# Kernel optimization log

Measured on AMD Instinct MI355X. Metric: run time of the kernel, lower is better.

The kernel has to match this reference:

```python
import jax, jax.numpy as jnp
import numpy as np

SCALE_EPS = 1e-05


def _qweight(weight):
    # global abs-mean scale (detached), round-to-nearest-even, clamp to {-1,0,1}
    scale = SCALE_EPS + jax.lax.stop_gradient(jnp.mean(jnp.abs(weight)))
    quant = jnp.clip(jnp.round(weight / scale), -1.0, 1.0)
    # straight-through estimator: forward = quant, backward = identity on weight
    return weight + jax.lax.stop_gradient(quant - weight)


def setup_inputs() -> dict:
    key = jax.random.key(0)
    k_x, k_w = jax.random.split(key)
    B, S, IN, OUT = 4, 2048, 2048, 8192
    x = jax.random.normal(k_x, (B, S, IN), dtype=jnp.float32)
    weight = jax.random.normal(k_w, (OUT, IN), dtype=jnp.float32)
    bias = jnp.zeros((OUT,), dtype=jnp.float32)
    return {"x": x, "weight": weight, "bias": bias}


def reference(x, weight, bias):
    qw = _qweight(weight)  # ternary-valued (scaled forward value)
    # F.linear: x @ qw.T + bias ; [b,s,in] x [out,in] -> [b,s,out]
    return jnp.einsum('bsi,oi->bso', x, qw) + bias
```

## Files before the change

kernel.cpp:

```cpp
#include <hip/hip_runtime.h>
#include <hip/hip_bf16.h>

typedef __attribute__((ext_vector_type(8))) short bf16x8;
typedef __attribute__((ext_vector_type(4))) float f32x4;

__device__ __forceinline__ unsigned short f2bf_rne(float f) {
  unsigned int u = __float_as_uint(f);
  u += 0x7FFFu + ((u >> 16) & 1u);
  return (unsigned short)(u >> 16);
}

__device__ __forceinline__ float bf2f(unsigned short h) {
  return __uint_as_float(((unsigned int)h) << 16);
}

__global__ void absmean_kernel(const float* __restrict__ w, long n, double* __restrict__ out) {
  double s = 0.0;
  long stride = (long)gridDim.x * blockDim.x * 4;
  for (long i = ((long)blockIdx.x * blockDim.x + threadIdx.x) * 4; i < n; i += stride) {
    float4 v = *(const float4*)(w + i);
    s += (double)fabsf(v.x) + (double)fabsf(v.y) + (double)fabsf(v.z) + (double)fabsf(v.w);
  }
  for (int o = 32; o > 0; o >>= 1) s += __shfl_down(s, o, 64);
  __shared__ double ls[4];
  int lane = threadIdx.x & 63, wv = threadIdx.x >> 6;
  if (lane == 0) ls[wv] = s;
  __syncthreads();
  if (threadIdx.x == 0) atomicAdd(out, ls[0] + ls[1] + ls[2] + ls[3]);
}

__global__ void prep_x_kernel(const float* __restrict__ x, unsigned short* __restrict__ xcat,
                              int kshift, long n) {
  const int K = 1 << kshift;
  long stride = (long)gridDim.x * blockDim.x * 4;
  for (long i = ((long)blockIdx.x * blockDim.x + threadIdx.x) * 4; i < n; i += stride) {
    float4 v = *(const float4*)(x + i);
    float f[4] = {v.x, v.y, v.z, v.w};
    unsigned short hi[4], lo[4];
#pragma unroll
    for (int j = 0; j < 4; ++j) {
      hi[j] = f2bf_rne(f[j]);
      lo[j] = f2bf_rne(f[j] - bf2f(hi[j]));
    }
    long row = i >> kshift;
    int col = (int)(i & (K - 1));
    unsigned short* p0 = xcat + (row << (kshift + 1)) + col;
    *(ushort4*)p0 = make_ushort4(hi[0], hi[1], hi[2], hi[3]);
    *(ushort4*)(p0 + K) = make_ushort4(lo[0], lo[1], lo[2], lo[3]);
  }
}

__global__ void prep_w_kernel(const float* __restrict__ w, unsigned short* __restrict__ wcat,
                              const double* __restrict__ sum, int kshift, long n,
                              double inv_cnt) {
  const int K = 1 << kshift;
  float scale = 1e-5f + (float)(*sum * inv_cnt);
  long stride = (long)gridDim.x * blockDim.x * 4;
  for (long i = ((long)blockIdx.x * blockDim.x + threadIdx.x) * 4; i < n; i += stride) {
    float4 v = *(const float4*)(w + i);
    float f[4] = {v.x, v.y, v.z, v.w};
    unsigned short q[4];
#pragma unroll
    for (int j = 0; j < 4; ++j) {
      float t = f[j] / scale;
      t = rintf(t);
      t = fminf(1.0f, fmaxf(-1.0f, t));
      q[j] = f2bf_rne(t);
    }
    long row = i >> kshift;
    int col = (int)(i & (K - 1));
    unsigned short* p0 = wcat + (row << (kshift + 1)) + col;
    *(ushort4*)p0 = make_ushort4(q[0], q[1], q[2], q[3]);
    *(ushort4*)(p0 + K) = make_ushort4(q[0], q[1], q[2], q[3]);
  }
}

__device__ __forceinline__ void gll16(const unsigned short* g, void* l) {
  __builtin_amdgcn_global_load_lds((const __attribute__((address_space(1))) unsigned int*)g,
                                   (__attribute__((address_space(3))) unsigned int*)l,
                                   16, 0, 0);
}

__global__ __launch_bounds__(512) void gemm8p_kernel(
    const unsigned short* __restrict__ A,
    const unsigned short* __restrict__ Bw,
    const float* __restrict__ bias,
    float* __restrict__ C, int M, int N) {
  constexpr int Kc = 4096;
  constexpr int NT = 128;
  __shared__ __align__(16) unsigned short lds[65536];

  const int nbx = N >> 8;
  const int nwg = (M >> 8) * nbx;
  const int q8 = nwg >> 3, r8 = nwg & 7;
  const int xcd = blockIdx.x & 7;
  const int loc = blockIdx.x >> 3;
  const int wgid = (xcd < r8 ? xcd * (q8 + 1) : r8 * (q8 + 1) + (xcd - r8) * q8) + loc;
  const int bx = wgid % nbx;
  const int by = wgid / nbx;
  const int bm = by << 8;
  const int bn = bx << 8;

  const int tid = threadIdx.x;
  const int lane = tid & 63;
  const int wid = tid >> 6;
  const int wr = wid >> 2;
  const int wc = wid & 3;

  f32x4 acc[8][4] = {};

  const int strow = tid >> 2;
  const int sslot = ((tid & 3) ^ ((tid >> 2) & 3)) * 8;
  const unsigned short* sA0 = A + (size_t)(bm + strow) * Kc + sslot;
  const unsigned short* sA1 = A + (size_t)(bm + 128 + strow) * Kc + sslot;
  const unsigned short* sB0 = Bw + (size_t)(bn + strow) * Kc + sslot;
  const unsigned short* sB1 = Bw + (size_t)(bn + 128 + strow) * Kc + sslot;
  char* dA = (char*)lds + (size_t)wid * 1024;
  char* dB = (char*)lds + 65536 + (size_t)wid * 1024;

  const int scol = (((lane >> 4) ^ (lane & 3)) << 3);
  const int aoff = (wr * 128 + (lane & 15)) * 32 + scol;
  const int boff = 32768 + (wc * 64 + (lane & 15)) * 32 + scol;

#pragma unroll
  for (int p = 0; p < 3; ++p) {
    gll16(sA0 + p * 32, dA + p * 16384);
    gll16(sA1 + p * 32, dA + p * 16384 + 8192);
    gll16(sB0 + p * 32, dB + p * 16384);
    gll16(sB1 + p * 32, dB + p * 16384 + 8192);
  }
  asm volatile("s_waitcnt vmcnt(8)" ::: "memory");
  __builtin_amdgcn_s_barrier();

  bf16x8 a_[4], b_[4];
  for (int t = 0; t < NT; ++t) {
    const unsigned short* base = lds + (t & 3) * 8192;
    const int sb = (t + 3) & 3;
    const int sk = (t + 3) * 32;
    const bool doStage = (t + 3) < NT;

#pragma unroll
    for (int mi = 0; mi < 4; ++mi)
      a_[mi] = *(const bf16x8*)&base[aoff + mi * 512];
#pragma unroll
    for (int ni = 0; ni < 4; ++ni)
      b_[ni] = *(const bf16x8*)&base[boff + ni * 512];
    if (doStage) {
      gll16(sA0 + sk, dA + sb * 16384);
      gll16(sA1 + sk, dA + sb * 16384 + 8192);
    }
    __builtin_amdgcn_s_barrier();
    asm volatile("s_waitcnt lgkmcnt(0)" ::: "memory");
    __builtin_amdgcn_sched_barrier(0);
    __builtin_amdgcn_s_setprio(1);
#pragma unroll
    for (int mi = 0; mi < 4; ++mi)
#pragma unroll
      for (int ni = 0; ni < 4; ++ni)
        acc[mi][ni] = __builtin_amdgcn_mfma_f32_16x16x32_bf16(a_[mi], b_[ni], acc[mi][ni], 0, 0, 0);
    __builtin_amdgcn_s_setprio(0);
    __builtin_amdgcn_s_barrier();

#pragma unroll
    for (int mi = 0; mi < 4; ++mi)
      a_[mi] = *(const bf16x8*)&base[aoff + (mi + 4) * 512];
    if (doStage) {
      gll16(sB0 + sk, dB + sb * 16384);
      gll16(sB1 + sk, dB + sb * 16384 + 8192);
    }
    __builtin_amdgcn_s_barrier();
    asm volatile("s_waitcnt lgkmcnt(0)" ::: "memory");
    __builtin_amdgcn_sched_barrier(0);
    __builtin_amdgcn_s_setprio(1);
#pragma unroll
    for (int mi = 0; mi < 4; ++mi)
#pragma unroll
      for (int ni = 0; ni < 4; ++ni)
        acc[mi + 4][ni] = __builtin_amdgcn_mfma_f32_16x16x32_bf16(a_[mi], b_[ni], acc[mi + 4][ni], 0, 0, 0);
    __builtin_amdgcn_s_setprio(0);
    if (t < NT - 3) {
      asm volatile("s_waitcnt vmcnt(8)" ::: "memory");
    } else if (t == NT - 3) {
      asm volatile("s_waitcnt vmcnt(4)" ::: "memory");
    } else if (t == NT - 2) {
      asm volatile("s_waitcnt vmcnt(0)" ::: "memory");
    }
    __builtin_amdgcn_s_barrier();
  }

  const int r0 = bm + wr * 128 + (lane >> 4) * 4;
  const int c0 = bn + wc * 64 + (lane & 15);
#pragma unroll
  for (int ni = 0; ni < 4; ++ni) {
    const int col = c0 + ni * 16;
    const float bv = bias[col];
#pragma unroll
    for (int mi = 0; mi < 8; ++mi) {
#pragma unroll
      for (int rr = 0; rr < 4; ++rr)
        C[(size_t)(r0 + mi * 16 + rr) * N + col] = acc[mi][ni][rr] + bv;
    }
  }
}

__global__ void fallback_kernel(const float* __restrict__ x, const float* __restrict__ w,
                                const float* __restrict__ bias, const double* __restrict__ sum,
                                float* __restrict__ out, int M, int N, int K, double inv_cnt) {
  float scale = 1e-5f + (float)(*sum * inv_cnt);
  __shared__ float xs[64][33];
  __shared__ float qs[64][33];
  const int tid = threadIdx.x;
  const int bm = blockIdx.y * 64, bn = blockIdx.x * 64;
  const int ty = tid >> 4, tx = tid & 15;
  float acc[4][4] = {};
  for (int k0 = 0; k0 < K; k0 += 32) {
    for (int p = 0; p < 8; ++p) {
      int idx = p * 256 + tid;
      int r = idx >> 5, c = idx & 31;
      xs[r][c] = x[(size_t)(bm + r) * K + k0 + c];
      float t = w[(size_t)(bn + r) * K + k0 + c] / scale;
      t = rintf(t);
      qs[r][c] = fminf(1.0f, fmaxf(-1.0f, t));
    }
    __syncthreads();
    for (int kk = 0; kk < 32; ++kk) {
      float a[4], b[4];
#pragma unroll
      for (int i = 0; i < 4; ++i) a[i] = xs[ty * 4 + i][kk];
#pragma unroll
      for (int j = 0; j < 4; ++j) b[j] = qs[tx * 4 + j][kk];
#pragma unroll
      for (int i = 0; i < 4; ++i)
#pragma unroll
        for (int j = 0; j < 4; ++j) acc[i][j] += a[i] * b[j];
    }
    __syncthreads();
  }
#pragma unroll
  for (int i = 0; i < 4; ++i)
#pragma unroll
    for (int j = 0; j < 4; ++j)
      out[(size_t)(bm + ty * 4 + i) * N + bn + tx * 4 + j] = acc[i][j] + bias[bn + tx * 4 + j];
}

extern "C" void kernel_launch(void* const* d_in, const int* in_sizes, int n_in,
                              void* d_out, int out_size, void* d_ws, size_t ws_size,
                              hipStream_t stream) {
  const float* x = (const float*)d_in[0];
  const float* w = (const float*)d_in[1];
  const float* bias = (const float*)d_in[2];
  float* out = (float*)d_out;

  const int K = 2048;
  const int kshift = 11;
  const int M = in_sizes[0] / K;
  const int N = in_sizes[2];
  const int Kc = 2 * K;
  const long nw = (long)N * K;
  const long nx = (long)M * K;
  const double inv_cnt = 1.0 / (double)nw;

  double* sum = (double*)d_ws;
  hipMemsetAsync(d_ws, 0, sizeof(double), stream);
  absmean_kernel<<<2048, 256, 0, stream>>>(w, nw, sum);

  size_t need = 256 + ((size_t)M + (size_t)N) * (size_t)Kc * sizeof(unsigned short);
  bool shapes_ok = (K == 2048) && ((M & 255) == 0) && ((N & 255) == 0);
  if (shapes_ok && ws_size >= need) {
    unsigned short* xcat = (unsigned short*)((char*)d_ws + 256);
    unsigned short* wcat = xcat + (size_t)M * Kc;
    prep_x_kernel<<<2048, 256, 0, stream>>>(x, xcat, kshift, nx);
    prep_w_kernel<<<2048, 256, 0, stream>>>(w, wcat, sum, kshift, nw, inv_cnt);
    int nwg = (M >> 8) * (N >> 8);
    gemm8p_kernel<<<nwg, 512, 0, stream>>>(xcat, wcat, bias, out, M, N);
  } else {
    dim3 grid(N / 64, M / 64);
    fallback_kernel<<<grid, 256, 0, stream>>>(x, w, bias, sum, out, M, N, K, inv_cnt);
  }
}
```

Measured before the change: 927.0 us.

## Restructure GEMM to K=64 tiles with double buffering instead of 4-stage K=32

The GEMM main loop now stages 64-wide K slices into two LDS buffers instead of 32-wide slices into four rotating buffers, which halves the iteration count. Each iteration runs four MFMA phases over the two K-halves. The LDS swizzle and the global-to-LDS staging pattern are changed to match. The aim is fewer barriers and loop overheads per unit of K and larger global loads. In exchange, prefetch depth drops to one tile ahead and every iteration ends with a full vmcnt(0) wait, which may expose memory latency.

```diff
diff --git a/kernel.cpp b/kernel.cpp
--- a/kernel.cpp
+++ b/kernel.cpp
@@ -81,13 +81,13 @@
                                    16, 0, 0);
 }
 
-__global__ __launch_bounds__(512) void gemm8p_kernel(
+__global__ __launch_bounds__(512) void gemm4p_kernel(
     const unsigned short* __restrict__ A,
     const unsigned short* __restrict__ Bw,
     const float* __restrict__ bias,
     float* __restrict__ C, int M, int N) {
   constexpr int Kc = 4096;
-  constexpr int NT = 128;
+  constexpr int NT = 64;
   __shared__ __align__(16) unsigned short lds[65536];
 
   const int nbx = N >> 8;
@@ -109,45 +109,41 @@
 
   f32x4 acc[8][4] = {};
 
-  const int strow = tid >> 2;
-  const int sslot = ((tid & 3) ^ ((tid >> 2) & 3)) * 8;
-  const unsigned short* sA0 = A + (size_t)(bm + strow) * Kc + sslot;
-  const unsigned short* sA1 = A + (size_t)(bm + 128 + strow) * Kc + sslot;
-  const unsigned short* sB0 = Bw + (size_t)(bn + strow) * Kc + sslot;
-  const unsigned short* sB1 = Bw + (size_t)(bn + 128 + strow) * Kc + sslot;
-  char* dA = (char*)lds + (size_t)wid * 1024;
-  char* dB = (char*)lds + 65536 + (size_t)wid * 1024;
-
-  const int scol = (((lane >> 4) ^ (lane & 3)) << 3);
-  const int aoff = (wr * 128 + (lane & 15)) * 32 + scol;
-  const int boff = 32768 + (wc * 64 + (lane & 15)) * 32 + scol;
-
-#pragma unroll
-  for (int p = 0; p < 3; ++p) {
-    gll16(sA0 + p * 32, dA + p * 16384);
-    gll16(sA1 + p * 32, dA + p * 16384 + 8192);
-    gll16(sB0 + p * 32, dB + p * 16384);
-    gll16(sB1 + p * 32, dB + p * 16384 + 8192);
-  }
-  asm volatile("s_waitcnt vmcnt(8)" ::: "memory");
+  const int strow = tid >> 3;
+  const int scole = ((tid & 7) * 8) ^ (((tid >> 5) & 1) * 16);
+  const unsigned short* sA = A + (size_t)(bm + strow) * Kc + scole;
+  const unsigned short* sB = Bw + (size_t)(bn + strow) * Kc + scole;
+  const size_t rj = (size_t)64 * Kc;
+  char* ldsb = (char*)lds;
+  char* dbase = ldsb + (size_t)wid * 1024;
+
+  const int swz = ((lane >> 4) * 8) ^ ((lane & 4) * 4);
+  const int aoff = wr * 8192 + (lane & 15) * 64 + swz;
+  const int boff = 32768 + wc * 4096 + (lane & 15) * 64 + swz;
+
+#pragma unroll
+  for (int j = 0; j < 4; ++j) {
+    gll16(sA + j * rj, dbase + j * 8192);
+    gll16(sB + j * rj, dbase + 65536 + j * 8192);
+  }
+  asm volatile("s_waitcnt vmcnt(0)" ::: "memory");
   __builtin_amdgcn_s_barrier();
 
   bf16x8 a_[4], b_[4];
   for (int t = 0; t < NT; ++t) {
-    const unsigned short* base = lds + (t & 3) * 8192;
-    const int sb = (t + 3) & 3;
-    const int sk = (t + 3) * 32;
-    const bool doStage = (t + 3) < NT;
-
-#pragma unroll
-    for (int mi = 0; mi < 4; ++mi)
-      a_[mi] = *(const bf16x8*)&base[aoff + mi * 512];
-#pragma unroll
-    for (int ni = 0; ni < 4; ++ni)
-      b_[ni] = *(const bf16x8*)&base[boff + ni * 512];
+    const int ab = aoff + (t & 1) * 16384;
+    const int bb = boff + (t & 1) * 16384;
+    const int sbuf = ((t + 1) & 1) * 32768;
+    const int sk = (t + 1) * 64;
+    const bool doStage = (t + 1) < NT;
+
+#pragma unroll
+    for (int mi = 0; mi < 4; ++mi) a_[mi] = *(const bf16x8*)&lds[ab + mi * 1024];
+#pragma unroll
+    for (int ni = 0; ni < 4; ++ni) b_[ni] = *(const bf16x8*)&lds[bb + ni * 1024];
     if (doStage) {
-      gll16(sA0 + sk, dA + sb * 16384);
-      gll16(sA1 + sk, dA + sb * 16384 + 8192);
+#pragma unroll
+      for (int j = 0; j < 4; ++j) gll16(sA + sk + j * rj, dbase + sbuf + j * 8192);
     }
     __builtin_amdgcn_s_barrier();
     asm volatile("s_waitcnt lgkmcnt(0)" ::: "memory");
@@ -162,11 +158,10 @@
     __builtin_amdgcn_s_barrier();
 
 #pragma unroll
-    for (int mi = 0; mi < 4; ++mi)
-      a_[mi] = *(const bf16x8*)&base[aoff + (mi + 4) * 512];
+    for (int mi = 0; mi < 4; ++mi) a_[mi] = *(const bf16x8*)&lds[ab + (mi + 4) * 1024];
     if (doStage) {
-      gll16(sB0 + sk, dB + sb * 16384);
-      gll16(sB1 + sk, dB + sb * 16384 + 8192);
+#pragma unroll
+      for (int j = 0; j < 4; ++j) gll16(sB + sk + j * rj, dbase + sbuf + 65536 + j * 8192);
     }
     __builtin_amdgcn_s_barrier();
     asm volatile("s_waitcnt lgkmcnt(0)" ::: "memory");
@@ -178,13 +173,37 @@
       for (int ni = 0; ni < 4; ++ni)
         acc[mi + 4][ni] = __builtin_amdgcn_mfma_f32_16x16x32_bf16(a_[mi], b_[ni], acc[mi + 4][ni], 0, 0, 0);
     __builtin_amdgcn_s_setprio(0);
-    if (t < NT - 3) {
-      asm volatile("s_waitcnt vmcnt(8)" ::: "memory");
-    } else if (t == NT - 3) {
-      asm volatile("s_waitcnt vmcnt(4)" ::: "memory");
-    } else if (t == NT - 2) {
-      asm volatile("s_waitcnt vmcnt(0)" ::: "memory");
-    }
+    __builtin_amdgcn_s_barrier();
+
+#pragma unroll
+    for (int mi = 0; mi < 4; ++mi) a_[mi] = *(const bf16x8*)&lds[ab + mi * 1024 + 32];
+#pragma unroll
+    for (int ni = 0; ni < 4; ++ni) b_[ni] = *(const bf16x8*)&lds[bb + ni * 1024 + 32];
+    __builtin_amdgcn_s_barrier();
+    asm volatile("s_waitcnt lgkmcnt(0)" ::: "memory");
+    __builtin_amdgcn_sched_barrier(0);
+    __builtin_amdgcn_s_setprio(1);
+#pragma unroll
+    for (int mi = 0; mi < 4; ++mi)
+#pragma unroll
+      for (int ni = 0; ni < 4; ++ni)
+        acc[mi][ni] = __builtin_amdgcn_mfma_f32_16x16x32_bf16(a_[mi], b_[ni], acc[mi][ni], 0, 0, 0);
+    __builtin_amdgcn_s_setprio(0);
+    __builtin_amdgcn_s_barrier();
+
+#pragma unroll
+    for (int mi = 0; mi < 4; ++mi) a_[mi] = *(const bf16x8*)&lds[ab + (mi + 4) * 1024 + 32];
+    asm volatile("s_waitcnt vmcnt(0)" ::: "memory");
+    __builtin_amdgcn_s_barrier();
+    asm volatile("s_waitcnt lgkmcnt(0)" ::: "memory");
+    __builtin_amdgcn_sched_barrier(0);
+    __builtin_amdgcn_s_setprio(1);
+#pragma unroll
+    for (int mi = 0; mi < 4; ++mi)
+#pragma unroll
+      for (int ni = 0; ni < 4; ++ni)
+        acc[mi + 4][ni] = __builtin_amdgcn_mfma_f32_16x16x32_bf16(a_[mi], b_[ni], acc[mi + 4][ni], 0, 0, 0);
+    __builtin_amdgcn_s_setprio(0);
     __builtin_amdgcn_s_barrier();
   }
 
@@ -272,7 +291,7 @@
     prep_x_kernel<<<2048, 256, 0, stream>>>(x, xcat, kshift, nx);
     prep_w_kernel<<<2048, 256, 0, stream>>>(w, wcat, sum, kshift, nw, inv_cnt);
     int nwg = (M >> 8) * (N >> 8);
-    gemm8p_kernel<<<nwg, 512, 0, stream>>>(xcat, wcat, bias, out, M, N);
+    gemm4p_kernel<<<nwg, 512, 0, stream>>>(xcat, wcat, bias, out, M, N);
   } else {
     dim3 grid(N / 64, M / 64);
     fallback_kernel<<<grid, 256, 0, stream>>>(x, w, bias, sum, out, M, N, K, inv_cnt);
```

Result: no change. 923.8 us (-0.4%).
